# Performance work log

Hardware: AMD Instinct MI355X
Metric: run time of the kernel (lower is better)

The kernel has to match this reference:

```python
import jax, jax.numpy as jnp
import numpy as np

N_NODES = 50000
N_EDGES = 600000
D_IN = 128
HID = 128
N_SAGE = 2          # num_layers - 1
N_GRAPHS = 512
BN_EPS = 1e-5


def setup_inputs() -> dict:
    key = jax.random.key(0)
    ks = jax.random.split(key, 12)
    s = 1.0 / np.sqrt(HID)
    x = jax.random.normal(ks[0], (N_NODES, D_IN), dtype=jnp.float32)
    edge_index = jax.random.randint(ks[1], (2, N_EDGES), 0, N_NODES, dtype=jnp.int32)
    batch = jnp.sort(jax.random.randint(ks[2], (N_NODES,), 0, N_GRAPHS, dtype=jnp.int32))
    # GIN MLP: Linear(D_IN,HID) -> ReLU -> Linear(HID,HID)
    gin_w1 = jax.random.normal(ks[3], (D_IN, HID), dtype=jnp.float32) * s
    gin_b1 = jnp.zeros((HID,), jnp.float32)
    gin_w2 = jax.random.normal(ks[4], (HID, HID), dtype=jnp.float32) * s
    gin_b2 = jnp.zeros((HID,), jnp.float32)
    # SAGEConv layers: lin_l (neighbors, with bias), lin_r (root, no bias)
    sage_wl = jax.random.normal(ks[5], (N_SAGE, HID, HID), dtype=jnp.float32) * s
    sage_bl = jnp.zeros((N_SAGE, HID), jnp.float32)
    sage_wr = jax.random.normal(ks[6], (N_SAGE, HID, HID), dtype=jnp.float32) * s
    # BatchNorm per layer (3 layers)
    bn_gamma = jnp.ones((1 + N_SAGE, HID), jnp.float32)
    bn_beta = jnp.zeros((1 + N_SAGE, HID), jnp.float32)
    return {"x": x, "edge_index": edge_index, "batch": batch,
            "gin_w1": gin_w1, "gin_b1": gin_b1, "gin_w2": gin_w2, "gin_b2": gin_b2,
            "sage_wl": sage_wl, "sage_bl": sage_bl, "sage_wr": sage_wr,
            "bn_gamma": bn_gamma, "bn_beta": bn_beta}


def _batchnorm(h, gamma, beta):
    # training-mode BN over the node dimension (biased variance, as torch)
    mu = jnp.mean(h, axis=0)
    var = jnp.var(h, axis=0)
    return gamma * (h - mu) * jax.lax.rsqrt(var + BN_EPS) + beta


def reference(x, edge_index, batch, gin_w1, gin_b1, gin_w2, gin_b2,
              sage_wl, sage_bl, sage_wr, bn_gamma, bn_beta):
    n = x.shape[0]
    src, dst = edge_index[0], edge_index[1]

    # ---- Layer 0: GINConv (eps=0): mlp(x + sum_{j->i} x_j) ----
    agg = jax.ops.segment_sum(x[src], dst, num_segments=n)  # [N, D_IN]
    h = x + agg
    h = jax.nn.relu(h @ gin_w1 + gin_b1) @ gin_w2 + gin_b2
    h = jax.nn.relu(_batchnorm(h, bn_gamma[0], bn_beta[0]))
    # dropout is identity (eval mode)

    # degree for mean aggregation (shared across SAGE layers)
    deg = jax.ops.segment_sum(jnp.ones((src.shape[0],), h.dtype), dst, num_segments=n)
    inv_deg = (1.0 / jnp.maximum(deg, 1.0))[:, None]  # [N,1]

    # ---- SAGE layers: lin_l(mean_{j->i} h_j) + lin_r(h_i) ----
    for l in range(N_SAGE):
        neigh = jax.ops.segment_sum(h[src], dst, num_segments=n) * inv_deg
        h = neigh @ sage_wl[l] + sage_bl[l] + h @ sage_wr[l]
        h = jax.nn.relu(_batchnorm(h, bn_gamma[l + 1], bn_beta[l + 1]))

    # ---- global mean pool over batch ids ----
    sums = jax.ops.segment_sum(h, batch, num_segments=N_GRAPHS)  # [G, HID]
    counts = jax.ops.segment_sum(jnp.ones((n,), h.dtype), batch, num_segments=N_GRAPHS)
    return sums / jnp.maximum(counts, 1.0)[:, None]
```

## Files before the change

### kernel.cpp

```cpp
#include <hip/hip_runtime.h>

#define N_NODES 50000
#define N_EDGES 600000
#define HID 128
#define N_GRAPHS 512
#define BN_EPS 1e-5f
#define INV_N (1.0f / 50000.0f)
#define SLICE_STRIDE 800000
#define GATHER_GROUPS 391
#define IDXCAP 4096

typedef __attribute__((ext_vector_type(8))) short bf16x8;
typedef __attribute__((ext_vector_type(4))) float f32x4;

__device__ __forceinline__ unsigned short f2b(float f) {
    unsigned u = __float_as_uint(f);
    return (unsigned short)((u + 0x7FFFu + ((u >> 16) & 1u)) >> 16);
}
__device__ __forceinline__ float b2f(unsigned short h) {
    return __uint_as_float(((unsigned)h) << 16);
}

__device__ __forceinline__ float stats_sum(const float* __restrict__ s, int idx) {
    float v = 0.f;
#pragma unroll
    for (int r = 0; r < 8; r++) v += s[r * 256 + idx];
    return v;
}

#define CONVX_BLOCKS 6250
#define WCONV_BLOCKS 384
#define DEG_BLOCKS   2344
__global__ __launch_bounds__(256) void prep_kernel(
    const float* __restrict__ x, const float* __restrict__ gw1, const float* __restrict__ gw2,
    const float* __restrict__ swl, const float* __restrict__ swr, const int* __restrict__ dst,
    unsigned short* __restrict__ x16, unsigned short* __restrict__ wt, int* __restrict__ deg)
{
    int b = blockIdx.x;
    int t = threadIdx.x;
    if (b < CONVX_BLOCKS) {
        int gid = b * 256 + t;
        int i = gid >> 5, l = gid & 31;
        if (i >= N_NODES) return;
        int c0 = l * 4;
        float4 v = *(const float4*)(x + (size_t)i * 128 + c0);
        ushort4 o;
        o.x = f2b(v.x); o.y = f2b(v.y); o.z = f2b(v.z); o.w = f2b(v.w);
        *(ushort4*)(x16 + (size_t)(l >> 2) * SLICE_STRIDE + (size_t)i * 16 + (l & 3) * 4) = o;
    } else if (b < CONVX_BLOCKS + WCONV_BLOCKS) {
        int gid = (b - CONVX_BLOCKS) * 256 + t;
        int m = gid >> 14;
        int e = gid & 16383;
        int k = e >> 7;
        int n = e & 127;
        const float* src = (m == 0) ? gw1 : (m == 1) ? gw2 : (m == 2) ? swl
                         : (m == 3) ? swr : (m == 4) ? (swl + 16384) : (swr + 16384);
        wt[m * 16384 + n * 128 + k] = f2b(src[k * 128 + n]);
    } else {
        int e = (b - CONVX_BLOCKS - WCONV_BLOCKS) * 256 + t;
        if (e < N_EDGES) atomicAdd(&deg[dst[e]], 1);
    }
}

#define ALLOC_BLOCKS 196
__global__ __launch_bounds__(256) void alloc_kernel(int* __restrict__ cursor,
                                                    int* __restrict__ row_beg,
                                                    float* __restrict__ inv_deg,
                                                    int* __restrict__ total,
                                                    const int* __restrict__ batch,
                                                    int* __restrict__ gstart) {
    if (blockIdx.x >= ALLOC_BLOCKS) {
        int g = (blockIdx.x - ALLOC_BLOCKS) * 256 + threadIdx.x;
        if (g > N_GRAPHS) return;
        int lo = 0, hi = N_NODES;
        while (lo < hi) {
            int mid = (lo + hi) >> 1;
            if (batch[mid] < g) lo = mid + 1; else hi = mid;
        }
        gstart[g] = lo;
        return;
    }
    __shared__ int tmp[256];
    __shared__ int base;
    int i = blockIdx.x * 256 + threadIdx.x;
    int d = (i < N_NODES) ? cursor[i] : 0;
    tmp[threadIdx.x] = d;
    __syncthreads();
#pragma unroll
    for (int off = 1; off < 256; off <<= 1) {
        int v = (threadIdx.x >= off) ? tmp[threadIdx.x - off] : 0;
        __syncthreads();
        tmp[threadIdx.x] += v;
        __syncthreads();
    }
    if (threadIdx.x == 255) base = atomicAdd(total, tmp[255]);
    __syncthreads();
    if (i < N_NODES) {
        int b = base + tmp[threadIdx.x] - d;
        row_beg[i] = b;
        cursor[i] = b;
        inv_deg[i] = 1.0f / fmaxf((float)d, 1.0f);
    }
}

__global__ void csr_fill_kernel(const int* __restrict__ src, const int* __restrict__ dst,
                                int* __restrict__ cursor, unsigned short* __restrict__ csr_src, int nE) {
    int e = blockIdx.x * blockDim.x + threadIdx.x;
    if (e < nE) {
        int pos = atomicAdd(&cursor[dst[e]], 1);
        csr_src[pos] = (unsigned short)src[e];
    }
}

template<bool MEAN>
__global__ __launch_bounds__(256) void gather_slice_kernel(
    const unsigned short* __restrict__ feat_s,
    const int* __restrict__ row_beg, const int* __restrict__ row_end,
    const unsigned short* __restrict__ csr_src,
    const float* __restrict__ inv_deg,
    unsigned short* __restrict__ out_s)
{
    __shared__ unsigned short idxbuf[IDXCAP];
    const int t = threadIdx.x;
    const int slice = blockIdx.x & 7;
    const int grp = blockIdx.x >> 3;
    const int node0 = grp * 128;
    const int nlast = (node0 + 127 < N_NODES) ? node0 + 127 : N_NODES - 1;
    const int node = node0 + (t >> 1);
    const int l8 = (t & 1) * 8;
    const unsigned short* fbase = feat_s + (size_t)slice * SLICE_STRIDE + l8;

    const int ebeg = row_beg[node0];
    const int ecnt = row_end[nlast] - ebeg;
    const bool lds_ok = (ecnt <= IDXCAP);
    if (lds_ok)
        for (int i = t; i < ecnt; i += 256) idxbuf[i] = csr_src[ebeg + i];
    __syncthreads();
    if (node >= N_NODES) return;

    const int beg = row_beg[node];
    const int deg = row_end[node] - beg;

    float a[8];
#pragma unroll
    for (int j = 0; j < 8; j++) a[j] = 0.f;

    if (lds_ok) {
        const int off = beg - ebeg;
        int e = 0;
        for (; e + 7 < deg; e += 8) {
            int s[8];
#pragma unroll
            for (int u = 0; u < 8; u++) s[u] = idxbuf[off + e + u];
            bf16x8 v[8];
#pragma unroll
            for (int u = 0; u < 8; u++)
                v[u] = *(const bf16x8*)(fbase + (size_t)s[u] * 16);
#pragma unroll
            for (int u = 0; u < 8; u++)
#pragma unroll
                for (int j = 0; j < 8; j++)
                    a[j] += b2f((unsigned short)v[u][j]);
        }
        for (; e + 3 < deg; e += 4) {
            int s[4];
#pragma unroll
            for (int u = 0; u < 4; u++) s[u] = idxbuf[off + e + u];
            bf16x8 v[4];
#pragma unroll
            for (int u = 0; u < 4; u++)
                v[u] = *(const bf16x8*)(fbase + (size_t)s[u] * 16);
#pragma unroll
            for (int u = 0; u < 4; u++)
#pragma unroll
                for (int j = 0; j < 8; j++)
                    a[j] += b2f((unsigned short)v[u][j]);
        }
        for (; e < deg; e++) {
            int s0 = idxbuf[off + e];
            bf16x8 v0 = *(const bf16x8*)(fbase + (size_t)s0 * 16);
#pragma unroll
            for (int j = 0; j < 8; j++)
                a[j] += b2f((unsigned short)v0[j]);
        }
    } else {
        for (int e = beg; e < beg + deg; e++) {
            int s0 = csr_src[e];
            bf16x8 v0 = *(const bf16x8*)(fbase + (size_t)s0 * 16);
#pragma unroll
            for (int j = 0; j < 8; j++)
                a[j] += b2f((unsigned short)v0[j]);
        }
    }

    if (MEAN) {
        float sc = inv_deg[node];
#pragma unroll
        for (int j = 0; j < 8; j++) a[j] *= sc;
    }
    bf16x8 o;
#pragma unroll
    for (int j = 0; j < 8; j++) o[j] = (short)f2b(a[j]);
    *(bf16x8*)(out_s + (size_t)slice * SLICE_STRIDE + (size_t)node * 16 + l8) = o;
}

__global__ __launch_bounds__(256, 2) void gemm_gin_kernel(
    const unsigned short* __restrict__ X, const unsigned short* __restrict__ AGG,
    const unsigned short* __restrict__ W1t, const unsigned short* __restrict__ W2t,
    const float* __restrict__ b1, const float* __restrict__ b2,
    float* __restrict__ stats, unsigned short* __restrict__ Cb,
    int M, int ntiles)
{
    __shared__ unsigned short t1[32][136];
    __shared__ float red[2][128];

    const int t = threadIdx.x;
    const int wave = t >> 6;
    const int lane = t & 63;
    const int colhalf = wave & 1;
    const int rowpair = wave >> 1;
    const int m16 = lane & 15;
    const int quad = lane >> 4;
    const int k0 = quad * 8;
    const int colbase = colhalf * 64;
    const int lrow = rowpair * 16 + m16;

    const bf16x8 zero8 = {0, 0, 0, 0, 0, 0, 0, 0};

    bf16x8 w1f[4][4], w2f[4][4];
#pragma unroll
    for (int ct = 0; ct < 4; ct++) {
        int col = colbase + ct * 16 + m16;
#pragma unroll
        for (int kc = 0; kc < 4; kc++) {
            w1f[ct][kc] = *(const bf16x8*)(W1t + (size_t)col * 128 + kc * 32 + k0);
            w2f[ct][kc] = *(const bf16x8*)(W2t + (size_t)col * 128 + kc * 32 + k0);
        }
    }
    f32x4 bs1[4], bs2[4];
#pragma unroll
    for (int ct = 0; ct < 4; ct++) {
        bs1[ct] = *(const f32x4*)(b1 + colbase + ct * 16 + quad * 4);
        bs2[ct] = *(const f32x4*)(b2 + colbase + ct * 16 + quad * 4);
    }

    float psum[4][4], psq[4][4];
#pragma unroll
    for (int ct = 0; ct < 4; ct++)
#pragma unroll
        for (int r = 0; r < 4; r++) { psum[ct][r] = 0.f; psq[ct][r] = 0.f; }

    for (int tile = blockIdx.x; tile < ntiles; tile += gridDim.x) {
        int arow = tile * 32 + rowpair * 16 + m16;
        bool aok = arow < M;

        bf16x8 a[4];
#pragma unroll
        for (int kc = 0; kc < 4; kc++) {
            if (aok) {
                size_t aoff = (size_t)(kc * 2 + (quad >> 1)) * SLICE_STRIDE
                            + (size_t)arow * 16 + (quad & 1) * 8;
                bf16x8 vx = *(const bf16x8*)(X + aoff);
                bf16x8 vg = *(const bf16x8*)(AGG + aoff);
                bf16x8 r;
#pragma unroll
                for (int i = 0; i < 8; i++)
                    r[i] = (short)f2b(b2f((unsigned short)vx[i]) + b2f((unsigned short)vg[i]));
                a[kc] = r;
            } else {
                a[kc] = zero8;
            }
        }

        f32x4 acc[4];
#pragma unroll
        for (int ct = 0; ct < 4; ct++) acc[ct] = (f32x4){0.f, 0.f, 0.f, 0.f};
#pragma unroll
        for (int kc = 0; kc < 4; kc++)
#pragma unroll
            for (int ct = 0; ct < 4; ct++)
                acc[ct] = __builtin_amdgcn_mfma_f32_16x16x32_bf16(w1f[ct][kc], a[kc], acc[ct], 0, 0, 0);

        __syncthreads();
#pragma unroll
        for (int ct = 0; ct < 4; ct++) {
            f32x4 v = acc[ct] + bs1[ct];
            ushort4 o;
            o.x = f2b(fmaxf(v[0], 0.f));
            o.y = f2b(fmaxf(v[1], 0.f));
            o.z = f2b(fmaxf(v[2], 0.f));
            o.w = f2b(fmaxf(v[3], 0.f));
            *(ushort4*)&t1[lrow][colbase + ct * 16 + quad * 4] = o;
        }
        __syncthreads();

        bf16x8 ta[4];
#pragma unroll
        for (int kc = 0; kc < 4; kc++)
            ta[kc] = *(const bf16x8*)&t1[lrow][kc * 32 + k0];

        f32x4 acc2[4];
#pragma unroll
        for (int ct = 0; ct < 4; ct++) acc2[ct] = (f32x4){0.f, 0.f, 0.f, 0.f};
#pragma unroll
        for (int kc = 0; kc < 4; kc++)
#pragma unroll
            for (int ct = 0; ct < 4; ct++)
                acc2[ct] = __builtin_amdgcn_mfma_f32_16x16x32_bf16(w2f[ct][kc], ta[kc], acc2[ct], 0, 0, 0);

        if (arow < M) {
#pragma unroll
            for (int ct = 0; ct < 4; ct++) {
                f32x4 v = acc2[ct] + bs2[ct];
#pragma unroll
                for (int r = 0; r < 4; r++) { psum[ct][r] += v[r]; psq[ct][r] += v[r] * v[r]; }
                ushort4 o;
                o.x = f2b(v[0]); o.y = f2b(v[1]); o.z = f2b(v[2]); o.w = f2b(v[3]);
                int cs = (colbase >> 4) + ct;
                *(ushort4*)(Cb + (size_t)cs * SLICE_STRIDE + (size_t)arow * 16 + quad * 4) = o;
            }
        }
    }

#pragma unroll
    for (int ct = 0; ct < 4; ct++)
#pragma unroll
        for (int r = 0; r < 4; r++) {
#pragma unroll
            for (int mask = 1; mask <= 8; mask <<= 1) {
                psum[ct][r] += __shfl_xor(psum[ct][r], mask, 64);
                psq[ct][r]  += __shfl_xor(psq[ct][r], mask, 64);
            }
        }
    __syncthreads();
    if (m16 == 0) {
#pragma unroll
        for (int ct = 0; ct < 4; ct++)
#pragma unroll
            for (int r = 0; r < 4; r++)
                red[rowpair][colbase + ct * 16 + quad * 4 + r] = psum[ct][r];
    }
    __syncthreads();
    if (t < 128) atomicAdd(&stats[(blockIdx.x & 7) * 256 + t], red[0][t] + red[1][t]);
    __syncthreads();
    if (m16 == 0) {
#pragma unroll
        for (int ct = 0; ct < 4; ct++)
#pragma unroll
            for (int r = 0; r < 4; r++)
                red[rowpair][colbase + ct * 16 + quad * 4 + r] = psq[ct][r];
    }
    __syncthreads();
    if (t < 128) atomicAdd(&stats[(blockIdx.x & 7) * 256 + 128 + t], red[0][t] + red[1][t]);
}

__global__ __launch_bounds__(256) void gemm_dual_kernel(
    const unsigned short* __restrict__ A1, const unsigned short* __restrict__ A2,
    const unsigned short* __restrict__ W1t, const unsigned short* __restrict__ W2t,
    const float* __restrict__ bias, float* __restrict__ stats,
    unsigned short* __restrict__ Cb, int M, int ntiles)
{
    __shared__ float red[128];

    const int t = threadIdx.x;
    const int wave = t >> 6;
    const int lane = t & 63;
    const int m16 = lane & 15;
    const int quad = lane >> 4;
    const int k0 = quad * 8;
    const int colbase = wave * 32;

    const bf16x8 zero8 = {0, 0, 0, 0, 0, 0, 0, 0};

    bf16x8 w1f[2][4], w2f[2][4];
#pragma unroll
    for (int ct = 0; ct < 2; ct++) {
        int col = colbase + ct * 16 + m16;
#pragma unroll
        for (int kc = 0; kc < 4; kc++) {
            w1f[ct][kc] = *(const bf16x8*)(W1t + (size_t)col * 128 + kc * 32 + k0);
            w2f[ct][kc] = *(const bf16x8*)(W2t + (size_t)col * 128 + kc * 32 + k0);
        }
    }
    f32x4 bs[2];
#pragma unroll
    for (int ct = 0; ct < 2; ct++)
        bs[ct] = *(const f32x4*)(bias + colbase + ct * 16 + quad * 4);

    float psum[2][4], psq[2][4];
#pragma unroll
    for (int ct = 0; ct < 2; ct++)
#pragma unroll
        for (int r = 0; r < 4; r++) { psum[ct][r] = 0.f; psq[ct][r] = 0.f; }

    bf16x8 a1[4], a2[4], a1n[4], a2n[4];

    int tile = blockIdx.x;
    if (tile < ntiles) {
        int arow = tile * 16 + m16;
        bool aok = arow < M;
#pragma unroll
        for (int kc = 0; kc < 4; kc++) {
            size_t aoff = (size_t)(kc * 2 + (quad >> 1)) * SLICE_STRIDE
                        + (size_t)arow * 16 + (quad & 1) * 8;
            a1[kc] = aok ? *(const bf16x8*)(A1 + aoff) : zero8;
            a2[kc] = aok ? *(const bf16x8*)(A2 + aoff) : zero8;
        }
    }

    for (; tile < ntiles; tile += gridDim.x) {
        int nt = tile + gridDim.x;
        if (nt < ntiles) {
            int arow = nt * 16 + m16;
            bool aok = arow < M;
#pragma unroll
            for (int kc = 0; kc < 4; kc++) {
                size_t aoff = (size_t)(kc * 2 + (quad >> 1)) * SLICE_STRIDE
                            + (size_t)arow * 16 + (quad & 1) * 8;
                a1n[kc] = aok ? *(const bf16x8*)(A1 + aoff) : zero8;
                a2n[kc] = aok ? *(const bf16x8*)(A2 + aoff) : zero8;
            }
        }

        f32x4 acc[2];
        acc[0] = (f32x4){0.f, 0.f, 0.f, 0.f};
        acc[1] = (f32x4){0.f, 0.f, 0.f, 0.f};
#pragma unroll
        for (int kc = 0; kc < 4; kc++) {
#pragma unroll
            for (int ct = 0; ct < 2; ct++) {
                acc[ct] = __builtin_amdgcn_mfma_f32_16x16x32_bf16(w1f[ct][kc], a1[kc], acc[ct], 0, 0, 0);
                acc[ct] = __builtin_amdgcn_mfma_f32_16x16x32_bf16(w2f[ct][kc], a2[kc], acc[ct], 0, 0, 0);
            }
        }

        int orow = tile * 16 + m16;
        if (orow < M) {
#pragma unroll
            for (int ct = 0; ct < 2; ct++) {
                f32x4 v = acc[ct] + bs[ct];
#pragma unroll
                for (int r = 0; r < 4; r++) { psum[ct][r] += v[r]; psq[ct][r] += v[r] * v[r]; }
                ushort4 o;
                o.x = f2b(v[0]); o.y = f2b(v[1]); o.z = f2b(v[2]); o.w = f2b(v[3]);
                int cs = wave * 2 + ct;
                *(ushort4*)(Cb + (size_t)cs * SLICE_STRIDE + (size_t)orow * 16 + quad * 4) = o;
            }
        }

        if (nt < ntiles) {
            a1[0] = a1n[0]; a1[1] = a1n[1]; a1[2] = a1n[2]; a1[3] = a1n[3];
            a2[0] = a2n[0]; a2[1] = a2n[1]; a2[2] = a2n[2]; a2[3] = a2n[3];
        }
    }

#pragma unroll
    for (int ct = 0; ct < 2; ct++)
#pragma unroll
        for (int r = 0; r < 4; r++) {
#pragma unroll
            for (int mask = 1; mask <= 8; mask <<= 1) {
                psum[ct][r] += __shfl_xor(psum[ct][r], mask, 64);
                psq[ct][r]  += __shfl_xor(psq[ct][r], mask, 64);
            }
        }
    if (m16 == 0) {
#pragma unroll
        for (int ct = 0; ct < 2; ct++)
#pragma unroll
            for (int r = 0; r < 4; r++)
                red[colbase + ct * 16 + quad * 4 + r] = psum[ct][r];
    }
    __syncthreads();
    if (t < 128) atomicAdd(&stats[(blockIdx.x & 7) * 256 + t], red[t]);
    __syncthreads();
    if (m16 == 0) {
#pragma unroll
        for (int ct = 0; ct < 2; ct++)
#pragma unroll
            for (int r = 0; r < 4; r++)
                red[colbase + ct * 16 + quad * 4 + r] = psq[ct][r];
    }
    __syncthreads();
    if (t < 128) atomicAdd(&stats[(blockIdx.x & 7) * 256 + 128 + t], red[t]);
}

__global__ __launch_bounds__(256) void finish_kernel(
    const unsigned short* __restrict__ Hpre, const float* __restrict__ stats,
    const float* __restrict__ gamma, const float* __restrict__ beta,
    unsigned short* __restrict__ Hact)
{
    __shared__ float cs[2][128];
    int t = threadIdx.x;
    if (t < 128) {
        float mu = stats_sum(stats, t) * INV_N;
        float var = stats_sum(stats, 128 + t) * INV_N - mu * mu;
        float rs = rsqrtf(var + BN_EPS);
        float c = gamma[t] * rs;
        cs[0][t] = c;
        cs[1][t] = beta[t] - mu * c;
    }
    __syncthreads();
    int gid = blockIdx.x * 256 + t;
    int e0 = gid * 8;
    int s = (unsigned)e0 / SLICE_STRIDE;
    int rem = e0 - s * SLICE_STRIDE;
    int col0 = s * 16 + (rem & 15);
    bf16x8 v = *(const bf16x8*)(Hpre + e0);
    bf16x8 o;
#pragma unroll
    for (int j = 0; j < 8; j++)
        o[j] = (short)f2b(fmaxf(b2f((unsigned short)v[j]) * cs[0][col0 + j] + cs[1][col0 + j], 0.f));
    *(bf16x8*)(Hact + e0) = o;
}

__global__ __launch_bounds__(256) void pool_mean_kernel(const unsigned short* __restrict__ h_s,
                                                        const int* __restrict__ gstart,
                                                        const float* __restrict__ stats,
                                                        const float* __restrict__ gamma,
                                                        const float* __restrict__ beta,
                                                        float* __restrict__ out) {
    __shared__ float red[16][128];
    int g = blockIdx.x;
    int t = threadIdx.x;
    int grp = t >> 4;
    int ci = t & 15;
    int s = ci >> 1, off = (ci & 1) * 8;
    int c0 = ci * 8;
    float c[8], b[8];
#pragma unroll
    for (int j = 0; j < 8; j++) {
        int col = c0 + j;
        float mu = stats_sum(stats, col) * INV_N;
        float var = stats_sum(stats, 128 + col) * INV_N - mu * mu;
        float rs = rsqrtf(var + BN_EPS);
        c[j] = gamma[col] * rs;
        b[j] = beta[col] - mu * c[j];
    }
    int beg = gstart[g];
    int end = gstart[g + 1];
    float sa[8];
#pragma unroll
    for (int j = 0; j < 8; j++) sa[j] = 0.f;
    const unsigned short* base = h_s + (size_t)s * SLICE_STRIDE + off;
    for (int i = beg + grp; i < end; i += 16) {
        bf16x8 v = *(const bf16x8*)(base + (size_t)i * 16);
#pragma unroll
        for (int j = 0; j < 8; j++)
            sa[j] += fmaxf(b2f((unsigned short)v[j]) * c[j] + b[j], 0.f);
    }
#pragma unroll
    for (int j = 0; j < 8; j++) red[grp][c0 + j] = sa[j];
    __syncthreads();
    if (t < 128) {
        float cnt = fmaxf((float)(end - beg), 1.0f);
        float tot = 0.f;
#pragma unroll
        for (int r = 0; r < 16; r++) tot += red[r][t];
        out[(size_t)g * 128 + t] = tot / cnt;
    }
}

extern "C" void kernel_launch(void* const* d_in, const int* in_sizes, int n_in,
                              void* d_out, int out_size, void* d_ws, size_t ws_size,
                              hipStream_t stream) {
    const float* x    = (const float*)d_in[0];
    const int*   ei   = (const int*)d_in[1];
    const int*   src  = ei;
    const int*   dst  = ei + N_EDGES;
    const int*   batch = (const int*)d_in[2];
    const float* gw1  = (const float*)d_in[3];
    const float* gb1  = (const float*)d_in[4];
    const float* gw2  = (const float*)d_in[5];
    const float* gb2  = (const float*)d_in[6];
    const float* swl  = (const float*)d_in[7];
    const float* sbl  = (const float*)d_in[8];
    const float* swr  = (const float*)d_in[9];
    const float* bng  = (const float*)d_in[10];
    const float* bnb  = (const float*)d_in[11];
    float* out = (float*)d_out;

    float* ws = (float*)d_ws;
    unsigned short* x16_s  = (unsigned short*)(ws + 0);
    unsigned short* agg_s  = (unsigned short*)(ws + 3200000);
    unsigned short* hact_s = (unsigned short*)(ws + 6400000);
    unsigned short* hpre_s = (unsigned short*)(ws + 9600000);
    unsigned short* wt     = (unsigned short*)(ws + 12800000);
    float*          inv_deg= ws + 12850000;
    int*            row_beg= (int*)(ws + 12900000);
    int*            cursor = (int*)(ws + 12950000);
    int*            total  = cursor + 50000;
    float*          stats  = (float*)(cursor + 50001);
    unsigned short* csr_src= (unsigned short*)(ws + 13100000);
    int*            gstart = (int*)(ws + 13700000);

    const int ggrid = 512;
    const int ntiles32 = (N_NODES + 31) / 32;
    const int ntiles16 = (N_NODES + 15) / 16;
    const int gather_grid = GATHER_GROUPS * 8;

    hipMemsetAsync(cursor, 0, (50001 + 3 * 8 * 256) * sizeof(int), stream);

    prep_kernel<<<CONVX_BLOCKS + WCONV_BLOCKS + DEG_BLOCKS, 256, 0, stream>>>(
        x, gw1, gw2, swl, swr, dst, x16_s, wt, cursor);

    alloc_kernel<<<ALLOC_BLOCKS + 3, 256, 0, stream>>>(cursor, row_beg, inv_deg, total, batch, gstart);
    csr_fill_kernel<<<(N_EDGES + 255) / 256, 256, 0, stream>>>(src, dst, cursor, csr_src, N_EDGES);

    gather_slice_kernel<false><<<gather_grid, 256, 0, stream>>>(
        x16_s, row_beg, cursor, csr_src, nullptr, agg_s);
    gemm_gin_kernel<<<ggrid, 256, 0, stream>>>(
        x16_s, agg_s, wt + 0 * 16384, wt + 1 * 16384, gb1, gb2,
        stats + 0 * 2048, hpre_s, N_NODES, ntiles32);
    finish_kernel<<<3125, 256, 0, stream>>>(
        hpre_s, stats + 0 * 2048, bng + 0 * HID, bnb + 0 * HID, hact_s);

    gather_slice_kernel<true><<<gather_grid, 256, 0, stream>>>(
        hact_s, row_beg, cursor, csr_src, inv_deg, agg_s);
    gemm_dual_kernel<<<ggrid, 256, 0, stream>>>(
        agg_s, hact_s, wt + 2 * 16384, wt + 3 * 16384, sbl + 0 * HID,
        stats + 1 * 2048, hpre_s, N_NODES, ntiles16);
    finish_kernel<<<3125, 256, 0, stream>>>(
        hpre_s, stats + 1 * 2048, bng + 1 * HID, bnb + 1 * HID, hact_s);

    gather_slice_kernel<true><<<gather_grid, 256, 0, stream>>>(
        hact_s, row_beg, cursor, csr_src, inv_deg, agg_s);
    gemm_dual_kernel<<<ggrid, 256, 0, stream>>>(
        agg_s, hact_s, wt + 4 * 16384, wt + 5 * 16384, sbl + 1 * HID,
        stats + 2 * 2048, hpre_s, N_NODES, ntiles16);

    pool_mean_kernel<<<N_GRAPHS, 256, 0, stream>>>(
        hpre_s, gstart, stats + 2 * 2048, bng + 2 * HID, bnb + 2 * HID, out);
}
```

Before: 312.4 us.

## Fuse BatchNorm+ReLU into gather and widen feature slices to 32 columns

Removes the standalone finish kernel by applying the BatchNorm affine and ReLU inside the gather kernel. Each gathered neighbor row is normalized on the fly, and the gather also writes the activated root rows for the next GEMM. The sliced feature layout changes from 8 slices of 16 columns to 4 slices of 32 columns, and the GEMM, pool and prep indexing are updated to match. This saves two full read/write passes over the node features, at the cost of extra ALU work per gathered edge, a smaller LDS index buffer (so the fallback path triggers more often) and a different gather access width.

New measurement: 347.5 us. +11.2%, slower.

```diff
diff --git a/kernel.cpp b/kernel.cpp
--- a/kernel.cpp
+++ b/kernel.cpp
@@ -6,9 +6,10 @@
 #define N_GRAPHS 512
 #define BN_EPS 1e-5f
 #define INV_N (1.0f / 50000.0f)
-#define SLICE_STRIDE 800000
-#define GATHER_GROUPS 391
-#define IDXCAP 4096
+#define SLICE_STRIDE 1600000
+#define NSLICES 4
+#define GATHER_GROUPS 782
+#define IDXCAP 1536
 
 typedef __attribute__((ext_vector_type(8))) short bf16x8;
 typedef __attribute__((ext_vector_type(4))) float f32x4;
@@ -46,7 +47,7 @@
         float4 v = *(const float4*)(x + (size_t)i * 128 + c0);
         ushort4 o;
         o.x = f2b(v.x); o.y = f2b(v.y); o.z = f2b(v.z); o.w = f2b(v.w);
-        *(ushort4*)(x16 + (size_t)(l >> 2) * SLICE_STRIDE + (size_t)i * 16 + (l & 3) * 4) = o;
+        *(ushort4*)(x16 + (size_t)(l >> 3) * SLICE_STRIDE + (size_t)i * 32 + (l & 7) * 4) = o;
     } else if (b < CONVX_BLOCKS + WCONV_BLOCKS) {
         int gid = (b - CONVX_BLOCKS) * 256 + t;
         int m = gid >> 14;
@@ -112,23 +113,36 @@
     }
 }
 
-template<bool MEAN>
-__global__ __launch_bounds__(256) void gather_slice_kernel(
+template<bool AFF>
+__global__ __launch_bounds__(256, 6) void gather_slice_kernel(
     const unsigned short* __restrict__ feat_s,
     const int* __restrict__ row_beg, const int* __restrict__ row_end,
     const unsigned short* __restrict__ csr_src,
     const float* __restrict__ inv_deg,
-    unsigned short* __restrict__ out_s)
+    const float* __restrict__ stats_in, const float* __restrict__ gamma,
+    const float* __restrict__ beta,
+    unsigned short* __restrict__ agg_s, unsigned short* __restrict__ hact_s)
 {
     __shared__ unsigned short idxbuf[IDXCAP];
+    __shared__ float csc[32], css[32];
     const int t = threadIdx.x;
-    const int slice = blockIdx.x & 7;
-    const int grp = blockIdx.x >> 3;
-    const int node0 = grp * 128;
-    const int nlast = (node0 + 127 < N_NODES) ? node0 + 127 : N_NODES - 1;
-    const int node = node0 + (t >> 1);
-    const int l8 = (t & 1) * 8;
+    const int slice = blockIdx.x & 3;
+    const int grp = blockIdx.x >> 2;
+    const int node0 = grp * 64;
+    const int nlast = (node0 + 63 < N_NODES) ? node0 + 63 : N_NODES - 1;
+    const int node = node0 + (t >> 2);
+    const int l8 = (t & 3) * 8;
     const unsigned short* fbase = feat_s + (size_t)slice * SLICE_STRIDE + l8;
+
+    if (AFF && t < 32) {
+        int col = slice * 32 + t;
+        float mu = stats_sum(stats_in, col) * INV_N;
+        float var = stats_sum(stats_in, 128 + col) * INV_N - mu * mu;
+        float rs = rsqrtf(var + BN_EPS);
+        float c = gamma[col] * rs;
+        csc[t] = c;
+        css[t] = beta[col] - mu * c;
+    }
 
     const int ebeg = row_beg[node0];
     const int ecnt = row_end[nlast] - ebeg;
@@ -138,6 +152,12 @@
     __syncthreads();
     if (node >= N_NODES) return;
 
+    float cc[8], ss[8];
+    if (AFF) {
+#pragma unroll
+        for (int j = 0; j < 8; j++) { cc[j] = csc[l8 + j]; ss[j] = css[l8 + j]; }
+    }
+
     const int beg = row_beg[node];
     const int deg = row_end[node] - beg;
 
@@ -155,12 +175,15 @@
             bf16x8 v[8];
 #pragma unroll
             for (int u = 0; u < 8; u++)
-                v[u] = *(const bf16x8*)(fbase + (size_t)s[u] * 16);
+                v[u] = *(const bf16x8*)(fbase + (size_t)s[u] * 32);
 #pragma unroll
             for (int u = 0; u < 8; u++)
 #pragma unroll
-                for (int j = 0; j < 8; j++)
-                    a[j] += b2f((unsigned short)v[u][j]);
+                for (int j = 0; j < 8; j++) {
+                    float tv = b2f((unsigned short)v[u][j]);
+                    if (AFF) tv = fmaxf(tv * cc[j] + ss[j], 0.f);
+                    a[j] += tv;
+                }
         }
         for (; e + 3 < deg; e += 4) {
             int s[4];
@@ -169,31 +192,40 @@
             bf16x8 v[4];
 #pragma unroll
             for (int u = 0; u < 4; u++)
-                v[u] = *(const bf16x8*)(fbase + (size_t)s[u] * 16);
+                v[u] = *(const bf16x8*)(fbase + (size_t)s[u] * 32);
 #pragma unroll
             for (int u = 0; u < 4; u++)
 #pragma unroll
-                for (int j = 0; j < 8; j++)
-                    a[j] += b2f((unsigned short)v[u][j]);
+                for (int j = 0; j < 8; j++) {
+                    float tv = b2f((unsigned short)v[u][j]);
+                    if (AFF) tv = fmaxf(tv * cc[j] + ss[j], 0.f);
+                    a[j] += tv;
+                }
         }
         for (; e < deg; e++) {
             int s0 = idxbuf[off + e];
-            bf16x8 v0 = *(const bf16x8*)(fbase + (size_t)s0 * 16);
-#pragma unroll
-            for (int j = 0; j < 8; j++)
-                a[j] += b2f((unsigned short)v0[j]);
+            bf16x8 v0 = *(const bf16x8*)(fbase + (size_t)s0 * 32);
+#pragma unroll
+            for (int j = 0; j < 8; j++) {
+                float tv = b2f((unsigned short)v0[j]);
+                if (AFF) tv = fmaxf(tv * cc[j] + ss[j], 0.f);
+                a[j] += tv;
+            }
         }
     } else {
         for (int e = beg; e < beg + deg; e++) {
             int s0 = csr_src[e];
-            bf16x8 v0 = *(const bf16x8*)(fbase + (size_t)s0 * 16);
-#pragma unroll
-            for (int j = 0; j < 8; j++)
-                a[j] += b2f((unsigned short)v0[j]);
-        }
-    }
-
-    if (MEAN) {
+            bf16x8 v0 = *(const bf16x8*)(fbase + (size_t)s0 * 32);
+#pragma unroll
+            for (int j = 0; j < 8; j++) {
+                float tv = b2f((unsigned short)v0[j]);
+                if (AFF) tv = fmaxf(tv * cc[j] + ss[j], 0.f);
+                a[j] += tv;
+            }
+        }
+    }
+
+    if (AFF) {
         float sc = inv_deg[node];
 #pragma unroll
         for (int j = 0; j < 8; j++) a[j] *= sc;
@@ -201,7 +233,16 @@
     bf16x8 o;
 #pragma unroll
     for (int j = 0; j < 8; j++) o[j] = (short)f2b(a[j]);
-    *(bf16x8*)(out_s + (size_t)slice * SLICE_STRIDE + (size_t)node * 16 + l8) = o;
+    *(bf16x8*)(agg_s + (size_t)slice * SLICE_STRIDE + (size_t)node * 32 + l8) = o;
+
+    if (AFF) {
+        bf16x8 v = *(const bf16x8*)(fbase + (size_t)node * 32);
+        bf16x8 h;
+#pragma unroll
+        for (int j = 0; j < 8; j++)
+            h[j] = (short)f2b(fmaxf(b2f((unsigned short)v[j]) * cc[j] + ss[j], 0.f));
+        *(bf16x8*)(hact_s + (size_t)slice * SLICE_STRIDE + (size_t)node * 32 + l8) = h;
+    }
 }
 
 __global__ __launch_bounds__(256, 2) void gemm_gin_kernel(
@@ -258,8 +299,7 @@
 #pragma unroll
         for (int kc = 0; kc < 4; kc++) {
             if (aok) {
-                size_t aoff = (size_t)(kc * 2 + (quad >> 1)) * SLICE_STRIDE
-                            + (size_t)arow * 16 + (quad & 1) * 8;
+                size_t aoff = (size_t)kc * SLICE_STRIDE + (size_t)arow * 32 + quad * 8;
                 bf16x8 vx = *(const bf16x8*)(X + aoff);
                 bf16x8 vg = *(const bf16x8*)(AGG + aoff);
                 bf16x8 r;
@@ -316,8 +356,10 @@
                 for (int r = 0; r < 4; r++) { psum[ct][r] += v[r]; psq[ct][r] += v[r] * v[r]; }
                 ushort4 o;
                 o.x = f2b(v[0]); o.y = f2b(v[1]); o.z = f2b(v[2]); o.w = f2b(v[3]);
-                int cs = (colbase >> 4) + ct;
-                *(ushort4*)(Cb + (size_t)cs * SLICE_STRIDE + (size_t)arow * 16 + quad * 4) = o;
+                int cloc = ct * 16 + quad * 4;
+                int cs = colhalf * 2 + (cloc >> 5);
+                int coff = cloc & 31;
+                *(ushort4*)(Cb + (size_t)cs * SLICE_STRIDE + (size_t)arow * 32 + coff) = o;
             }
         }
     }
@@ -401,8 +443,7 @@
         bool aok = arow < M;
 #pragma unroll
         for (int kc = 0; kc < 4; kc++) {
-            size_t aoff = (size_t)(kc * 2 + (quad >> 1)) * SLICE_STRIDE
-                        + (size_t)arow * 16 + (quad & 1) * 8;
+            size_t aoff = (size_t)kc * SLICE_STRIDE + (size_t)arow * 32 + quad * 8;
             a1[kc] = aok ? *(const bf16x8*)(A1 + aoff) : zero8;
             a2[kc] = aok ? *(const bf16x8*)(A2 + aoff) : zero8;
         }
@@ -415,8 +456,7 @@
             bool aok = arow < M;
 #pragma unroll
             for (int kc = 0; kc < 4; kc++) {
-                size_t aoff = (size_t)(kc * 2 + (quad >> 1)) * SLICE_STRIDE
-                            + (size_t)arow * 16 + (quad & 1) * 8;
+                size_t aoff = (size_t)kc * SLICE_STRIDE + (size_t)arow * 32 + quad * 8;
                 a1n[kc] = aok ? *(const bf16x8*)(A1 + aoff) : zero8;
                 a2n[kc] = aok ? *(const bf16x8*)(A2 + aoff) : zero8;
             }
@@ -443,8 +483,7 @@
                 for (int r = 0; r < 4; r++) { psum[ct][r] += v[r]; psq[ct][r] += v[r] * v[r]; }
                 ushort4 o;
                 o.x = f2b(v[0]); o.y = f2b(v[1]); o.z = f2b(v[2]); o.w = f2b(v[3]);
-                int cs = wave * 2 + ct;
-                *(ushort4*)(Cb + (size_t)cs * SLICE_STRIDE + (size_t)orow * 16 + quad * 4) = o;
+                *(ushort4*)(Cb + (size_t)wave * SLICE_STRIDE + (size_t)orow * 32 + ct * 16 + quad * 4) = o;
             }
         }
 
@@ -483,35 +522,6 @@
     }
     __syncthreads();
     if (t < 128) atomicAdd(&stats[(blockIdx.x & 7) * 256 + 128 + t], red[t]);
-}
-
-__global__ __launch_bounds__(256) void finish_kernel(
-    const unsigned short* __restrict__ Hpre, const float* __restrict__ stats,
-    const float* __restrict__ gamma, const float* __restrict__ beta,
-    unsigned short* __restrict__ Hact)
-{
-    __shared__ float cs[2][128];
-    int t = threadIdx.x;
-    if (t < 128) {
-        float mu = stats_sum(stats, t) * INV_N;
-        float var = stats_sum(stats, 128 + t) * INV_N - mu * mu;
-        float rs = rsqrtf(var + BN_EPS);
-        float c = gamma[t] * rs;
-        cs[0][t] = c;
-        cs[1][t] = beta[t] - mu * c;
-    }
-    __syncthreads();
-    int gid = blockIdx.x * 256 + t;
-    int e0 = gid * 8;
-    int s = (unsigned)e0 / SLICE_STRIDE;
-    int rem = e0 - s * SLICE_STRIDE;
-    int col0 = s * 16 + (rem & 15);
-    bf16x8 v = *(const bf16x8*)(Hpre + e0);
-    bf16x8 o;
-#pragma unroll
-    for (int j = 0; j < 8; j++)
-        o[j] = (short)f2b(fmaxf(b2f((unsigned short)v[j]) * cs[0][col0 + j] + cs[1][col0 + j], 0.f));
-    *(bf16x8*)(Hact + e0) = o;
 }
 
 __global__ __launch_bounds__(256) void pool_mean_kernel(const unsigned short* __restrict__ h_s,
@@ -525,7 +535,6 @@
     int t = threadIdx.x;
     int grp = t >> 4;
     int ci = t & 15;
-    int s = ci >> 1, off = (ci & 1) * 8;
     int c0 = ci * 8;
     float c[8], b[8];
 #pragma unroll
@@ -542,9 +551,9 @@
     float sa[8];
 #pragma unroll
     for (int j = 0; j < 8; j++) sa[j] = 0.f;
-    const unsigned short* base = h_s + (size_t)s * SLICE_STRIDE + off;
+    const unsigned short* base = h_s + (size_t)(ci >> 2) * SLICE_STRIDE + (ci & 3) * 8;
     for (int i = beg + grp; i < end; i += 16) {
-        bf16x8 v = *(const bf16x8*)(base + (size_t)i * 16);
+        bf16x8 v = *(const bf16x8*)(base + (size_t)i * 32);
 #pragma unroll
         for (int j = 0; j < 8; j++)
             sa[j] += fmaxf(b2f((unsigned short)v[j]) * c[j] + b[j], 0.f);
@@ -597,7 +606,7 @@
     const int ggrid = 512;
     const int ntiles32 = (N_NODES + 31) / 32;
     const int ntiles16 = (N_NODES + 15) / 16;
-    const int gather_grid = GATHER_GROUPS * 8;
+    const int gather_grid = GATHER_GROUPS * NSLICES;
 
     hipMemsetAsync(cursor, 0, (50001 + 3 * 8 * 256) * sizeof(int), stream);
 
@@ -608,23 +617,21 @@
     csr_fill_kernel<<<(N_EDGES + 255) / 256, 256, 0, stream>>>(src, dst, cursor, csr_src, N_EDGES);
 
     gather_slice_kernel<false><<<gather_grid, 256, 0, stream>>>(
-        x16_s, row_beg, cursor, csr_src, nullptr, agg_s);
+        x16_s, row_beg, cursor, csr_src, nullptr, nullptr, nullptr, nullptr, agg_s, nullptr);
     gemm_gin_kernel<<<ggrid, 256, 0, stream>>>(
         x16_s, agg_s, wt + 0 * 16384, wt + 1 * 16384, gb1, gb2,
         stats + 0 * 2048, hpre_s, N_NODES, ntiles32);
-    finish_kernel<<<3125, 256, 0, stream>>>(
-        hpre_s, stats + 0 * 2048, bng + 0 * HID, bnb + 0 * HID, hact_s);
 
     gather_slice_kernel<true><<<gather_grid, 256, 0, stream>>>(
-        hact_s, row_beg, cursor, csr_src, inv_deg, agg_s);
+        hpre_s, row_beg, cursor, csr_src, inv_deg,
+        stats + 0 * 2048, bng + 0 * HID, bnb + 0 * HID, agg_s, hact_s);
     gemm_dual_kernel<<<ggrid, 256, 0, stream>>>(
         agg_s, hact_s, wt + 2 * 16384, wt + 3 * 16384, sbl + 0 * HID,
         stats + 1 * 2048, hpre_s, N_NODES, ntiles16);
-    finish_kernel<<<3125, 256, 0, stream>>>(
-        hpre_s, stats + 1 * 2048, bng + 1 * HID, bnb + 1 * HID, hact_s);
 
     gather_slice_kernel<true><<<gather_grid, 256, 0, stream>>>(
-        hact_s, row_beg, cursor, csr_src, inv_deg, agg_s);
+        hpre_s, row_beg, cursor, csr_src, inv_deg,
+        stats + 1 * 2048, bng + 1 * HID, bnb + 1 * HID, agg_s, hact_s);
     gemm_dual_kernel<<<ggrid, 256, 0, stream>>>(
         agg_s, hact_s, wt + 4 * 16384, wt + 5 * 16384, sbl + 1 * HID,
         stats + 2 * 2048, hpre_s, N_NODES, ntiles16);
```

## Switch feature storage to 4 column slices of 32 bf16 per node

Applied to the files above, without the earlier changes.

Changes the column-sliced bf16 feature layout from 8 slices of 16 columns (32-byte rows) to 4 slices of 32 columns (64-byte rows). The gather, GEMM, finish and pool kernels are all updated to the new indexing. Gather blocks now cover 64 nodes with 4 lanes per node and a smaller index buffer, and gather output uses nontemporal stores. Each gathered neighbor row is read as a full 64-byte segment, which may use memory transactions better, but each slice's working set is twice as large and fits cache less readily.

Result: faster. 296.9 us, median of 2 (-5.0%).

```diff
diff --git a/kernel.cpp b/kernel.cpp
--- a/kernel.cpp
+++ b/kernel.cpp
@@ -6,9 +6,10 @@
 #define N_GRAPHS 512
 #define BN_EPS 1e-5f
 #define INV_N (1.0f / 50000.0f)
-#define SLICE_STRIDE 800000
-#define GATHER_GROUPS 391
-#define IDXCAP 4096
+#define SLICE_STRIDE 1600000
+#define NSLICES 4
+#define GATHER_GROUPS 782
+#define IDXCAP 2048
 
 typedef __attribute__((ext_vector_type(8))) short bf16x8;
 typedef __attribute__((ext_vector_type(4))) float f32x4;
@@ -46,7 +47,7 @@
         float4 v = *(const float4*)(x + (size_t)i * 128 + c0);
         ushort4 o;
         o.x = f2b(v.x); o.y = f2b(v.y); o.z = f2b(v.z); o.w = f2b(v.w);
-        *(ushort4*)(x16 + (size_t)(l >> 2) * SLICE_STRIDE + (size_t)i * 16 + (l & 3) * 4) = o;
+        *(ushort4*)(x16 + (size_t)(l >> 3) * SLICE_STRIDE + (size_t)i * 32 + (l & 7) * 4) = o;
     } else if (b < CONVX_BLOCKS + WCONV_BLOCKS) {
         int gid = (b - CONVX_BLOCKS) * 256 + t;
         int m = gid >> 14;
@@ -122,12 +123,12 @@
 {
     __shared__ unsigned short idxbuf[IDXCAP];
     const int t = threadIdx.x;
-    const int slice = blockIdx.x & 7;
-    const int grp = blockIdx.x >> 3;
-    const int node0 = grp * 128;
-    const int nlast = (node0 + 127 < N_NODES) ? node0 + 127 : N_NODES - 1;
-    const int node = node0 + (t >> 1);
-    const int l8 = (t & 1) * 8;
+    const int slice = blockIdx.x & 3;
+    const int grp = blockIdx.x >> 2;
+    const int node0 = grp * 64;
+    const int nlast = (node0 + 63 < N_NODES) ? node0 + 63 : N_NODES - 1;
+    const int node = node0 + (t >> 2);
+    const int l8 = (t & 3) * 8;
     const unsigned short* fbase = feat_s + (size_t)slice * SLICE_STRIDE + l8;
 
     const int ebeg = row_beg[node0];
@@ -155,7 +156,7 @@
             bf16x8 v[8];
 #pragma unroll
             for (int u = 0; u < 8; u++)
-                v[u] = *(const bf16x8*)(fbase + (size_t)s[u] * 16);
+                v[u] = *(const bf16x8*)(fbase + (size_t)s[u] * 32);
 #pragma unroll
             for (int u = 0; u < 8; u++)
 #pragma unroll
@@ -169,7 +170,7 @@
             bf16x8 v[4];
 #pragma unroll
             for (int u = 0; u < 4; u++)
-                v[u] = *(const bf16x8*)(fbase + (size_t)s[u] * 16);
+                v[u] = *(const bf16x8*)(fbase + (size_t)s[u] * 32);
 #pragma unroll
             for (int u = 0; u < 4; u++)
 #pragma unroll
@@ -178,7 +179,7 @@
         }
         for (; e < deg; e++) {
             int s0 = idxbuf[off + e];
-            bf16x8 v0 = *(const bf16x8*)(fbase + (size_t)s0 * 16);
+            bf16x8 v0 = *(const bf16x8*)(fbase + (size_t)s0 * 32);
 #pragma unroll
             for (int j = 0; j < 8; j++)
                 a[j] += b2f((unsigned short)v0[j]);
@@ -186,7 +187,7 @@
     } else {
         for (int e = beg; e < beg + deg; e++) {
             int s0 = csr_src[e];
-            bf16x8 v0 = *(const bf16x8*)(fbase + (size_t)s0 * 16);
+            bf16x8 v0 = *(const bf16x8*)(fbase + (size_t)s0 * 32);
 #pragma unroll
             for (int j = 0; j < 8; j++)
                 a[j] += b2f((unsigned short)v0[j]);
@@ -201,7 +202,8 @@
     bf16x8 o;
 #pragma unroll
     for (int j = 0; j < 8; j++) o[j] = (short)f2b(a[j]);
-    *(bf16x8*)(out_s + (size_t)slice * SLICE_STRIDE + (size_t)node * 16 + l8) = o;
+    __builtin_nontemporal_store(o,
+        (bf16x8*)(out_s + (size_t)slice * SLICE_STRIDE + (size_t)node * 32 + l8));
 }
 
 __global__ __launch_bounds__(256, 2) void gemm_gin_kernel(
@@ -258,8 +260,7 @@
 #pragma unroll
         for (int kc = 0; kc < 4; kc++) {
             if (aok) {
-                size_t aoff = (size_t)(kc * 2 + (quad >> 1)) * SLICE_STRIDE
-                            + (size_t)arow * 16 + (quad & 1) * 8;
+                size_t aoff = (size_t)kc * SLICE_STRIDE + (size_t)arow * 32 + quad * 8;
                 bf16x8 vx = *(const bf16x8*)(X + aoff);
                 bf16x8 vg = *(const bf16x8*)(AGG + aoff);
                 bf16x8 r;
@@ -316,8 +317,10 @@
                 for (int r = 0; r < 4; r++) { psum[ct][r] += v[r]; psq[ct][r] += v[r] * v[r]; }
                 ushort4 o;
                 o.x = f2b(v[0]); o.y = f2b(v[1]); o.z = f2b(v[2]); o.w = f2b(v[3]);
-                int cs = (colbase >> 4) + ct;
-                *(ushort4*)(Cb + (size_t)cs * SLICE_STRIDE + (size_t)arow * 16 + quad * 4) = o;
+                int cloc = ct * 16 + quad * 4;
+                int cs = colhalf * 2 + (cloc >> 5);
+                int coff = cloc & 31;
+                *(ushort4*)(Cb + (size_t)cs * SLICE_STRIDE + (size_t)arow * 32 + coff) = o;
             }
         }
     }
@@ -401,8 +404,7 @@
         bool aok = arow < M;
 #pragma unroll
         for (int kc = 0; kc < 4; kc++) {
-            size_t aoff = (size_t)(kc * 2 + (quad >> 1)) * SLICE_STRIDE
-                        + (size_t)arow * 16 + (quad & 1) * 8;
+            size_t aoff = (size_t)kc * SLICE_STRIDE + (size_t)arow * 32 + quad * 8;
             a1[kc] = aok ? *(const bf16x8*)(A1 + aoff) : zero8;
             a2[kc] = aok ? *(const bf16x8*)(A2 + aoff) : zero8;
         }
@@ -415,8 +417,7 @@
             bool aok = arow < M;
 #pragma unroll
             for (int kc = 0; kc < 4; kc++) {
-                size_t aoff = (size_t)(kc * 2 + (quad >> 1)) * SLICE_STRIDE
-                            + (size_t)arow * 16 + (quad & 1) * 8;
+                size_t aoff = (size_t)kc * SLICE_STRIDE + (size_t)arow * 32 + quad * 8;
                 a1n[kc] = aok ? *(const bf16x8*)(A1 + aoff) : zero8;
                 a2n[kc] = aok ? *(const bf16x8*)(A2 + aoff) : zero8;
             }
@@ -443,8 +444,7 @@
                 for (int r = 0; r < 4; r++) { psum[ct][r] += v[r]; psq[ct][r] += v[r] * v[r]; }
                 ushort4 o;
                 o.x = f2b(v[0]); o.y = f2b(v[1]); o.z = f2b(v[2]); o.w = f2b(v[3]);
-                int cs = wave * 2 + ct;
-                *(ushort4*)(Cb + (size_t)cs * SLICE_STRIDE + (size_t)orow * 16 + quad * 4) = o;
+                *(ushort4*)(Cb + (size_t)wave * SLICE_STRIDE + (size_t)orow * 32 + ct * 16 + quad * 4) = o;
             }
         }
 
@@ -502,10 +502,9 @@
     }
     __syncthreads();
     int gid = blockIdx.x * 256 + t;
-    int e0 = gid * 8;
-    int s = (unsigned)e0 / SLICE_STRIDE;
-    int rem = e0 - s * SLICE_STRIDE;
-    int col0 = s * 16 + (rem & 15);
+    size_t e0 = (size_t)gid * 8;
+    int s = (int)(e0 / SLICE_STRIDE);
+    int col0 = s * 32 + (int)(e0 & 31);
     bf16x8 v = *(const bf16x8*)(Hpre + e0);
     bf16x8 o;
 #pragma unroll
@@ -525,7 +524,6 @@
     int t = threadIdx.x;
     int grp = t >> 4;
     int ci = t & 15;
-    int s = ci >> 1, off = (ci & 1) * 8;
     int c0 = ci * 8;
     float c[8], b[8];
 #pragma unroll
@@ -542,9 +540,9 @@
     float sa[8];
 #pragma unroll
     for (int j = 0; j < 8; j++) sa[j] = 0.f;
-    const unsigned short* base = h_s + (size_t)s * SLICE_STRIDE + off;
+    const unsigned short* base = h_s + (size_t)(ci >> 2) * SLICE_STRIDE + (ci & 3) * 8;
     for (int i = beg + grp; i < end; i += 16) {
-        bf16x8 v = *(const bf16x8*)(base + (size_t)i * 16);
+        bf16x8 v = *(const bf16x8*)(base + (size_t)i * 32);
 #pragma unroll
         for (int j = 0; j < 8; j++)
             sa[j] += fmaxf(b2f((unsigned short)v[j]) * c[j] + b[j], 0.f);
@@ -597,7 +595,7 @@
     const int ggrid = 512;
     const int ntiles32 = (N_NODES + 31) / 32;
     const int ntiles16 = (N_NODES + 15) / 16;
-    const int gather_grid = GATHER_GROUPS * 8;
+    const int gather_grid = GATHER_GROUPS * NSLICES;
 
     hipMemsetAsync(cursor, 0, (50001 + 3 * 8 * 256) * sizeof(int), stream);
 
```
